# Kernel optimization log

Measured on AMD Instinct MI355X. Metric: run time of the kernel, lower is better.

Reference implementation:

```python
import jax, jax.numpy as jnp
import numpy as np

O, T = 20000, 80000
DIN_OBJ, DIN_PRED = 128, 128
H, DOUT = 256, 256
NCAPS, NHID = 8, 64
NLAYER, ROUTIT, TAU = 2, 3, 1.0
D = NCAPS * NHID                 # 512, routed feature dim
NFEAT1 = 2 * DIN_OBJ + DIN_PRED  # 384
NCLASS1 = 2 * H + DOUT           # 768
BN_EPS = 1e-5


def _l2norm(x):
    # torch fn.normalize(dim=-1): x / max(||x||, 1e-12)
    nrm = jnp.sqrt(jnp.sum(x * x, axis=-1, keepdims=True))
    return x / jnp.maximum(nrm, 1e-12)


def _rout(x, src, trg):
    # NeibRoutLayer: iterative capsule routing over edges
    n, d = x.shape
    dd = d // NCAPS
    x3 = _l2norm(x.reshape(n, NCAPS, dd))   # [n,k,dd]
    z = x3[src]                              # [m,k,dd] gathered source capsules
    u = x3
    for _ in range(ROUTIT):
        p = jax.nn.softmax(jnp.einsum('mkd,mkd->mk', z, u[trg]) / TAU, axis=1)  # [m,k]
        agg = jax.ops.segment_sum(z * p[:, :, None], trg, num_segments=n)       # scatter_add
        u = _l2norm(agg + x3)
    return u.reshape(n, d)


def _disengcn(x, src, trg, pca_w, pca_b, clf_w, clf_b, bn_g, bn_b):
    x = jax.nn.leaky_relu(x @ pca_w + pca_b)  # slope 0.01, dropout=0 (eval)
    for _ in range(NLAYER):
        x = _rout(x, src, trg)
    x = x @ clf_w + clf_b
    # BatchNorm1d in eval mode with running_mean=0, running_var=1
    x = x * (bn_g / jnp.sqrt(jnp.asarray(1.0 + BN_EPS, x.dtype))) + bn_b
    return jax.nn.leaky_relu(x)


def setup_inputs() -> dict:
    key = jax.random.key(0)
    ks = jax.random.split(key, 16)

    def unif(k, shape, stdv):
        return jax.random.uniform(k, shape, jnp.float32, -stdv, stdv)

    inp = {}
    inp['obj_vecs'] = jax.random.normal(ks[0], (O, DIN_OBJ), jnp.float32)
    inp['pred_vecs'] = jax.random.normal(ks[1], (T, DIN_PRED), jnp.float32)
    inp['edges'] = jax.random.randint(ks[2], (T, 2), 0, O, jnp.int64)
    # net1 params (SparseInputLinear uses 1/sqrt(out_dim), nn.Linear 1/sqrt(in_dim))
    inp['pca_w1'] = unif(ks[3], (NFEAT1, D), 1.0 / np.sqrt(D))
    inp['pca_b1'] = unif(ks[4], (D,), 1.0 / np.sqrt(D))
    inp['clf_w1'] = unif(ks[5], (D, NCLASS1), 1.0 / np.sqrt(D))
    inp['clf_b1'] = unif(ks[6], (NCLASS1,), 1.0 / np.sqrt(D))
    inp['bn_g1'] = 1.0 + 0.05 * jax.random.normal(ks[7], (NCLASS1,), jnp.float32)
    inp['bn_b1'] = 0.05 * jax.random.normal(ks[8], (NCLASS1,), jnp.float32)
    # net2 params
    inp['pca_w2'] = unif(ks[9], (H, D), 1.0 / np.sqrt(D))
    inp['pca_b2'] = unif(ks[10], (D,), 1.0 / np.sqrt(D))
    inp['clf_w2'] = unif(ks[11], (D, DOUT), 1.0 / np.sqrt(D))
    inp['clf_b2'] = unif(ks[12], (DOUT,), 1.0 / np.sqrt(D))
    inp['bn_g2'] = 1.0 + 0.05 * jax.random.normal(ks[13], (DOUT,), jnp.float32)
    inp['bn_b2'] = 0.05 * jax.random.normal(ks[14], (DOUT,), jnp.float32)
    return inp


def reference(obj_vecs, pred_vecs, edges, pca_w1, pca_b1, clf_w1, clf_b1, bn_g1, bn_b1,
              pca_w2, pca_b2, clf_w2, clf_b2, bn_g2, bn_b2):
    s_idx, o_idx = edges[:, 0], edges[:, 1]
    # extract_info: per-triplet concat [subj, pred, obj]
    t_vecs = jnp.concatenate([obj_vecs[s_idx], pred_vecs, obj_vecs[o_idx]], axis=1)  # [T, 384]
    out1 = _disengcn(t_vecs, s_idx, o_idx, pca_w1, pca_b1, clf_w1, clf_b1, bn_g1, bn_b1)  # [T, 768]
    # pool_objs: scatter_add subject/object features back to nodes, mean by count
    new_s = out1[:, :H]
    pred_out = out1[:, H:H + DOUT]
    new_o = out1[:, H + DOUT:]
    pooled = jax.ops.segment_sum(new_s, s_idx, num_segments=O) + \
             jax.ops.segment_sum(new_o, o_idx, num_segments=O)
    ones = jnp.ones((edges.shape[0],), out1.dtype)
    counts = jax.ops.segment_sum(ones, s_idx, num_segments=O) + \
             jax.ops.segment_sum(ones, o_idx, num_segments=O)
    pooled = pooled / jnp.maximum(counts, 1.0)[:, None]
    obj_out = _disengcn(pooled, s_idx, o_idx, pca_w2, pca_b2, clf_w2, clf_b2, bn_g2, bn_b2)  # [O, 256]
    return obj_out, pred_out
```

## Files before the change

### kernel.cpp

```cpp
#include <hip/hip_runtime.h>
#include <math.h>


#define O_N 20000
#define T_N 80000

typedef unsigned short bf_t;
typedef bf_t bfx8 __attribute__((ext_vector_type(8)));
typedef __attribute__((ext_vector_type(4))) float f32x4;
typedef __attribute__((ext_vector_type(8))) short s16x8;

#define AS1 __attribute__((address_space(1)))
#define AS3 __attribute__((address_space(3)))

__device__ __forceinline__ float leaky(float y) { return y > 0.0f ? y : 0.01f * y; }
__device__ __forceinline__ float bf2f(bf_t u) {
  union { unsigned int i; float f; } v; v.i = ((unsigned int)u) << 16; return v.f;
}
__device__ __forceinline__ bf_t f2bf(float f) {
  union { float f; unsigned int i; } v; v.f = f;
  unsigned int b = v.i;
  return (bf_t)((b + 0x7FFFu + ((b >> 16) & 1u)) >> 16);
}
__device__ __forceinline__ void gload16(const bf_t* g, bf_t* l) {
  __builtin_amdgcn_global_load_lds((const AS1 void*)g, (AS3 void*)l, 16, 0, 0);
}

__global__ void count_kernel(const int* __restrict__ edges, int* cnt_s, int* cnt_o) {
  int m = blockIdx.x * blockDim.x + threadIdx.x;
  if (m < T_N) {
    atomicAdd(&cnt_s[edges[2 * m]], 1);
    atomicAdd(&cnt_o[edges[2 * m + 1]], 1);
  }
}

__global__ void scan_kernel(const int* __restrict__ cnt_s, const int* __restrict__ cnt_o,
                            int* offs_s, int* offs_o, int* cur_o) {
  const int n = O_N;
  const int* cnt = (blockIdx.x == 0) ? cnt_s : cnt_o;
  int* offs = (blockIdx.x == 0) ? offs_s : offs_o;
  int* cur  = (blockIdx.x == 0) ? nullptr : cur_o;
  __shared__ int lds[1024];
  __shared__ int sbase;
  if (threadIdx.x == 0) sbase = 0;
  __syncthreads();
  for (int start = 0; start < n; start += 1024) {
    int i = start + (int)threadIdx.x;
    int v = (i < n) ? cnt[i] : 0;
    lds[threadIdx.x] = v;
    __syncthreads();
    for (int off = 1; off < 1024; off <<= 1) {
      int t = (threadIdx.x >= (unsigned)off) ? lds[threadIdx.x - off] : 0;
      __syncthreads();
      lds[threadIdx.x] += t;
      __syncthreads();
    }
    int base = sbase;
    int excl = base + lds[threadIdx.x] - v;
    if (i < n) { offs[i] = excl; if (cur) cur[i] = excl; }
    __syncthreads();
    if (threadIdx.x == 1023) sbase = base + lds[1023];
    __syncthreads();
  }
  if (threadIdx.x == 0) offs[n] = sbase;
}

__global__ void fill_kernel(const int* __restrict__ edges, int* cur_o, int* srcs) {
  int m = blockIdx.x * blockDim.x + threadIdx.x;
  if (m < T_N) {
    int s = edges[2 * m], o = edges[2 * m + 1];
    srcs[atomicAdd(&cur_o[o], 1)] = s;
  }
}

__global__ void transpose_cvt(const float* __restrict__ W, bf_t* __restrict__ Wt, int K, int N) {
  __shared__ float t[32][33];
  int kb = blockIdx.y << 5, nb = blockIdx.x << 5;
  int tx = threadIdx.x, ty = threadIdx.y;
#pragma unroll
  for (int r = 0; r < 32; r += 8) t[ty + r][tx] = W[(size_t)(kb + ty + r) * N + nb + tx];
  __syncthreads();
#pragma unroll
  for (int r = 0; r < 32; r += 8) Wt[(size_t)(nb + ty + r) * K + kb + tx] = f2bf(t[tx][ty + r]);
}

template <int MODE>
__global__ __launch_bounds__(256) void gemm_mfma(
    const bf_t* __restrict__ Ah, const bf_t* __restrict__ Axh,
    const float* __restrict__ Af,
    const float* __restrict__ obj, const float* __restrict__ pred,
    const int* __restrict__ edges,
    const bf_t* __restrict__ Wt, const float* __restrict__ bias,
    const float* __restrict__ bng, const float* __restrict__ bnb,
    bf_t* __restrict__ outh, float* __restrict__ outf, float* __restrict__ pool,
    int M, int N, int K) {
  constexpr bool REG = (MODE == 0 || MODE == 2);
  constexpr int ASTR = REG ? 40 : 32;
  __shared__ __align__(16) bf_t As[128 * ASTR];
  __shared__ __align__(16) bf_t Bs[128 * 32];
  __shared__ int sE[256];

  const int tid = threadIdx.x;
  const int w = tid >> 6, l = tid & 63;
  const int wr = w >> 1, wc = w & 1;
  const int row0 = blockIdx.y * 128, col0 = blockIdx.x * 128;

  const int srow = l >> 2;
  const int skb = ((l & 3) ^ ((l >> 2) & 3) ^ ((l >> 4) & 3)) * 8;
  const bf_t* pB[2];
  bf_t* ldsB[2];
  bf_t* ldsA[2];
  const bf_t* pA[2];
#pragma unroll
  for (int j = 0; j < 2; ++j) {
    int n = col0 + j * 64 + w * 16 + srow;
    pB[j] = Wt + (size_t)n * K + skb;
    ldsB[j] = Bs + (j * 64 + w * 16) * 32;
    ldsA[j] = As + (j * 64 + w * 16) * 32;
  }
  if constexpr (MODE == 1 || MODE == 3) {
#pragma unroll
    for (int j = 0; j < 2; ++j) {
      int m = row0 + j * 64 + w * 16 + srow;
      if (MODE == 3) m = min(m, M - 1);
      const bf_t* base = (MODE == 1) ? ((m < O_N) ? Ah : Axh) : Ah;
      pA[j] = base + (size_t)m * 512 + skb;
    }
  }
  int sIdx = 0, oIdx = 0, mrow = 0;
  if constexpr (MODE == 0) {
    mrow = row0 + (tid >> 1);
    sIdx = edges[2 * mrow];
    oIdx = edges[2 * mrow + 1];
  }
  if constexpr (MODE == 2) mrow = min(row0 + (tid >> 1), M - 1);
  if constexpr (MODE == 1) sE[tid] = edges[2 * row0 + tid];

  const int pkb = ((l >> 4) ^ (l & 3) ^ ((l >> 2) & 3)) * 8;
  int aoff[4], boff[4];
#pragma unroll
  for (int i = 0; i < 4; ++i) {
    int ar = wr * 64 + i * 16 + (l & 15);
    aoff[i] = REG ? (ar * 40 + (l >> 4) * 8) : (ar * 32 + pkb);
    int bn = wc * 64 + i * 16 + (l & 15);
    boff[i] = bn * 32 + pkb;
  }

  f32x4 acc[4][4];
  const f32x4 z4 = {0.f, 0.f, 0.f, 0.f};
#pragma unroll
  for (int i = 0; i < 4; ++i)
#pragma unroll
    for (int j = 0; j < 4; ++j) acc[i][j] = z4;

  for (int k0 = 0; k0 < K; k0 += 32) {
    if (k0) __syncthreads();
#pragma unroll
    for (int j = 0; j < 2; ++j) { gload16(pB[j], ldsB[j]); pB[j] += 32; }
    if constexpr (MODE == 1 || MODE == 3) {
#pragma unroll
      for (int j = 0; j < 2; ++j) { gload16(pA[j], ldsA[j]); pA[j] += 32; }
    } else {
      int r = tid >> 1, h = tid & 1;
      int c = k0 + h * 16;
      const float* base;
      if constexpr (MODE == 0) {
        if (c < 128)      base = obj  + (size_t)sIdx * 128 + c;
        else if (c < 256) base = pred + (size_t)mrow * 128 + (c - 128);
        else              base = obj  + (size_t)oIdx * 128 + (c - 256);
      } else {
        base = Af + (size_t)mrow * K + c;
      }
      float4 q0 = ((const float4*)base)[0];
      float4 q1 = ((const float4*)base)[1];
      float4 q2 = ((const float4*)base)[2];
      float4 q3 = ((const float4*)base)[3];
      bf_t* d = As + r * 40 + h * 16;
      bfx8 w0, w1;
      w0[0] = f2bf(q0.x); w0[1] = f2bf(q0.y); w0[2] = f2bf(q0.z); w0[3] = f2bf(q0.w);
      w0[4] = f2bf(q1.x); w0[5] = f2bf(q1.y); w0[6] = f2bf(q1.z); w0[7] = f2bf(q1.w);
      w1[0] = f2bf(q2.x); w1[1] = f2bf(q2.y); w1[2] = f2bf(q2.z); w1[3] = f2bf(q2.w);
      w1[4] = f2bf(q3.x); w1[5] = f2bf(q3.y); w1[6] = f2bf(q3.z); w1[7] = f2bf(q3.w);
      *(bfx8*)d = w0;
      *(bfx8*)(d + 8) = w1;
    }
    __syncthreads();
    s16x8 a[4], b[4];
#pragma unroll
    for (int i = 0; i < 4; ++i) a[i] = *(const s16x8*)(As + aoff[i]);
#pragma unroll
    for (int i = 0; i < 4; ++i) b[i] = *(const s16x8*)(Bs + boff[i]);
#pragma unroll
    for (int mi = 0; mi < 4; ++mi)
#pragma unroll
      for (int ni = 0; ni < 4; ++ni)
        acc[mi][ni] = __builtin_amdgcn_mfma_f32_16x16x32_bf16(a[mi], b[ni], acc[mi][ni], 0, 0, 0);
  }

  const int lg = l >> 4, li = l & 15;
  const float invs = 1.0f / sqrtf(1.0f + 1e-5f);
  int ncol[4];
  float bsv[4], bgv[4], bbv[4];
#pragma unroll
  for (int ni = 0; ni < 4; ++ni) {
    int n = col0 + wc * 64 + ni * 16 + li;
    ncol[ni] = n;
    bsv[ni] = bias[n];
    if constexpr (MODE == 1 || MODE == 3) { bgv[ni] = bng[n] * invs; bbv[ni] = bnb[n]; }
  }
  if constexpr (MODE == 0 || MODE == 2) {
#pragma unroll
    for (int mi = 0; mi < 4; ++mi) {
#pragma unroll
      for (int rg = 0; rg < 4; ++rg) {
        int m = row0 + wr * 64 + mi * 16 + lg * 4 + rg;
        float y[4], ssq = 0.f;
#pragma unroll
        for (int ni = 0; ni < 4; ++ni) {
          float v = leaky(acc[mi][ni][rg] + bsv[ni]);
          y[ni] = v; ssq += v * v;
        }
        ssq += __shfl_xor(ssq, 1); ssq += __shfl_xor(ssq, 2);
        ssq += __shfl_xor(ssq, 4); ssq += __shfl_xor(ssq, 8);
        if (MODE == 2 && m >= M) continue;
        float inv = 1.0f / fmaxf(sqrtf(ssq), 1e-12f);
#pragma unroll
        for (int ni = 0; ni < 4; ++ni)
          outh[(size_t)m * 512 + ncol[ni]] = f2bf(y[ni] * inv);
      }
    }
  } else if constexpr (MODE == 1) {
#pragma unroll
    for (int mi = 0; mi < 4; ++mi) {
#pragma unroll
      for (int rg = 0; rg < 4; ++rg) {
        int rloc = wr * 64 + mi * 16 + lg * 4 + rg;
        int m = row0 + rloc;
        int sI = sE[2 * rloc], oI = sE[2 * rloc + 1];
#pragma unroll
        for (int ni = 0; ni < 4; ++ni) {
          int n = ncol[ni];
          float v = leaky((acc[mi][ni][rg] + bsv[ni]) * bgv[ni] + bbv[ni]);
          if (n < 256)      atomicAdd(&pool[(size_t)sI * 256 + n], v);
          else if (n < 512) outf[(size_t)m * 256 + (n - 256)] = v;
          else              atomicAdd(&pool[(size_t)oI * 256 + (n - 512)], v);
        }
      }
    }
  } else {
#pragma unroll
    for (int mi = 0; mi < 4; ++mi) {
#pragma unroll
      for (int rg = 0; rg < 4; ++rg) {
        int m = row0 + wr * 64 + mi * 16 + lg * 4 + rg;
        if (m >= M) continue;
#pragma unroll
        for (int ni = 0; ni < 4; ++ni) {
          float v = leaky((acc[mi][ni][rg] + bsv[ni]) * bgv[ni] + bbv[ni]);
          outf[(size_t)m * 256 + ncol[ni]] = v;
        }
      }
    }
  }
}

__global__ __launch_bounds__(256) void rout_layer(
    const bf_t* __restrict__ Z, bf_t* __restrict__ U,
    const int* __restrict__ offs, const int* __restrict__ srcs, int nnodes) {
  int v = blockIdx.x * 4 + ((int)threadIdx.x >> 6);
  int lane = threadIdx.x & 63;
  if (v >= nnodes) return;
  bfx8 xv = *(const bfx8*)(Z + (size_t)v * 512 + lane * 8);
  float xr[8], ur[8];
#pragma unroll
  for (int q = 0; q < 8; ++q) { xr[q] = bf2f(xv[q]); ur[q] = xr[q]; }
  int e0 = offs[v], e1 = offs[v + 1];
  for (int it = 0; it < 3; ++it) {
    float ag[8] = {0, 0, 0, 0, 0, 0, 0, 0};
    for (int e = e0; e < e1; ++e) {
      bfx8 zv = *(const bfx8*)(Z + (size_t)srcs[e] * 512 + lane * 8);
      float zr[8];
      float d = 0.0f;
#pragma unroll
      for (int q = 0; q < 8; ++q) { zr[q] = bf2f(zv[q]); d += zr[q] * ur[q]; }
      d += __shfl_xor(d, 1); d += __shfl_xor(d, 2); d += __shfl_xor(d, 4);
      float mx = d;
      mx = fmaxf(mx, __shfl_xor(mx, 8));
      mx = fmaxf(mx, __shfl_xor(mx, 16));
      mx = fmaxf(mx, __shfl_xor(mx, 32));
      float ex = expf(d - mx);
      float sm = ex;
      sm += __shfl_xor(sm, 8); sm += __shfl_xor(sm, 16); sm += __shfl_xor(sm, 32);
      float pk = ex / sm;
#pragma unroll
      for (int q = 0; q < 8; ++q) ag[q] += pk * zr[q];
    }
    float ss = 0.0f, wv[8];
#pragma unroll
    for (int q = 0; q < 8; ++q) { wv[q] = ag[q] + xr[q]; ss += wv[q] * wv[q]; }
    ss += __shfl_xor(ss, 1); ss += __shfl_xor(ss, 2); ss += __shfl_xor(ss, 4);
    float inv = 1.0f / fmaxf(sqrtf(ss), 1e-12f);
#pragma unroll
    for (int q = 0; q < 8; ++q) ur[q] = wv[q] * inv;
  }
  bfx8 ov;
#pragma unroll
  for (int q = 0; q < 8; ++q) ov[q] = f2bf(ur[q]);
  *(bfx8*)(U + (size_t)v * 512 + lane * 8) = ov;
}

__global__ void divide_kernel(float* __restrict__ PL,
                              const int* __restrict__ offs_s, const int* __restrict__ offs_o) {
  int v = blockIdx.x;
  int c = threadIdx.x;
  float cnt = (float)((offs_s[v + 1] - offs_s[v]) + (offs_o[v + 1] - offs_o[v]));
  PL[(size_t)v * 256 + c] *= 1.0f / fmaxf(cnt, 1.0f);
}

extern "C" void kernel_launch(void* const* d_in, const int* in_sizes, int n_in,
                              void* d_out, int out_size, void* d_ws, size_t ws_size,
                              hipStream_t stream) {
  const float* obj    = (const float*)d_in[0];
  const float* pred   = (const float*)d_in[1];
  const int*   edges  = (const int*)d_in[2];
  const float* pca_w1 = (const float*)d_in[3];
  const float* pca_b1 = (const float*)d_in[4];
  const float* clf_w1 = (const float*)d_in[5];
  const float* clf_b1 = (const float*)d_in[6];
  const float* bn_g1  = (const float*)d_in[7];
  const float* bn_b1  = (const float*)d_in[8];
  const float* pca_w2 = (const float*)d_in[9];
  const float* pca_b2 = (const float*)d_in[10];
  const float* clf_w2 = (const float*)d_in[11];
  const float* clf_b2 = (const float*)d_in[12];
  const float* bn_g2  = (const float*)d_in[13];
  const float* bn_b2  = (const float*)d_in[14];
  float* outp = (float*)d_out;

  char* ws = (char*)d_ws;
  bf_t* Xh   = (bf_t*)ws;
  bf_t* Uh2  = (bf_t*)(ws + 81920000);
  float* PL  = (float*)(ws + 102400000);
  bf_t* Uh1  = (bf_t*)(ws + 102400000);
  bf_t* Wt1  = (bf_t*)(ws + 122880000);
  bf_t* Wt2  = (bf_t*)(ws + 123273216);
  bf_t* Wt3  = (bf_t*)(ws + 124059648);
  bf_t* Wt4  = (bf_t*)(ws + 124321792);
  int* I     = (int*)(ws + 124583936);
  int* cnt_s  = I;            int* cnt_o  = I + 20000;
  int* offs_s = I + 40000;    int* offs_o = I + 60001;
  int* cur_o  = I + 80002;    int* srcs   = I + 100002;

  hipMemsetAsync(cnt_s, 0, 160000, stream);
  count_kernel<<<313, 256, 0, stream>>>(edges, cnt_s, cnt_o);
  scan_kernel<<<2, 1024, 0, stream>>>(cnt_s, cnt_o, offs_s, offs_o, cur_o);
  fill_kernel<<<313, 256, 0, stream>>>(edges, cur_o, srcs);

  transpose_cvt<<<dim3(16, 12), dim3(32, 8), 0, stream>>>(pca_w1, Wt1, 384, 512);
  transpose_cvt<<<dim3(24, 16), dim3(32, 8), 0, stream>>>(clf_w1, Wt2, 512, 768);
  transpose_cvt<<<dim3(16, 8),  dim3(32, 8), 0, stream>>>(pca_w2, Wt3, 256, 512);
  transpose_cvt<<<dim3(8, 16),  dim3(32, 8), 0, stream>>>(clf_w2, Wt4, 512, 256);

  gemm_mfma<0><<<dim3(4, 625), 256, 0, stream>>>(nullptr, nullptr, nullptr, obj, pred, edges,
                                                 Wt1, pca_b1, nullptr, nullptr,
                                                 Xh, nullptr, nullptr, T_N, 512, 384);
  rout_layer<<<5000, 256, 0, stream>>>(Xh, Uh1, offs_o, srcs, O_N);
  rout_layer<<<5000, 256, 0, stream>>>(Uh1, Uh2, offs_o, srcs, O_N);
  hipMemsetAsync(PL, 0, 20480000, stream);
  gemm_mfma<1><<<dim3(6, 625), 256, 0, stream>>>(Uh2, Xh, nullptr, nullptr, nullptr, edges,
                                                 Wt2, clf_b1, bn_g1, bn_b1,
                                                 nullptr, outp + 5120000, PL, T_N, 768, 512);
  divide_kernel<<<O_N, 256, 0, stream>>>(PL, offs_s, offs_o);

  gemm_mfma<2><<<dim3(4, 157), 256, 0, stream>>>(nullptr, nullptr, PL, nullptr, nullptr, nullptr,
                                                 Wt3, pca_b2, nullptr, nullptr,
                                                 Xh, nullptr, nullptr, O_N, 512, 256);
  rout_layer<<<5000, 256, 0, stream>>>(Xh, Uh1, offs_o, srcs, O_N);
  rout_layer<<<5000, 256, 0, stream>>>(Uh1, Uh2, offs_o, srcs, O_N);
  gemm_mfma<3><<<dim3(2, 157), 256, 0, stream>>>(Uh2, nullptr, nullptr, nullptr, nullptr, nullptr,
                                                 Wt4, clf_b2, bn_g2, bn_b2,
                                                 nullptr, outp, nullptr, O_N, 256, 512);
}
```

Baseline: 773.3 us.

## Replace atomic pooling with CSR slot writes, pre-convert pred, cache rout sources

Several ideas land together. The pooling after the first DisenGCN now has the classifier GEMM write bf16 subject/object slices into CSR-ordered slots, and a gather kernel sums and averages them per node. This replaces float atomics, a memset and a divide kernel, but only when the workspace is large enough. pred_vecs is converted to bf16 once so the first GEMM can stream that segment with direct-to-LDS loads, and the register-staged A path switches to a swizzled 32-stride LDS layout. Routing caches up to 8 neighbour source rows in registers across the 3 iterations instead of re-reading them each time.

```diff
diff --git a/kernel.cpp b/kernel.cpp
--- a/kernel.cpp
+++ b/kernel.cpp
@@ -4,8 +4,10 @@
 
 #define O_N 20000
 #define T_N 80000
+#define BIG_REQ 207944000ull
 
 typedef unsigned short bf_t;
+typedef bf_t bfx4 __attribute__((ext_vector_type(4)));
 typedef bf_t bfx8 __attribute__((ext_vector_type(8)));
 typedef __attribute__((ext_vector_type(4))) float f32x4;
 typedef __attribute__((ext_vector_type(8))) short s16x8;
@@ -35,11 +37,11 @@
 }
 
 __global__ void scan_kernel(const int* __restrict__ cnt_s, const int* __restrict__ cnt_o,
-                            int* offs_s, int* offs_o, int* cur_o) {
+                            int* offs_s, int* cur_s, int* offs_o, int* cur_o) {
   const int n = O_N;
   const int* cnt = (blockIdx.x == 0) ? cnt_s : cnt_o;
   int* offs = (blockIdx.x == 0) ? offs_s : offs_o;
-  int* cur  = (blockIdx.x == 0) ? nullptr : cur_o;
+  int* cur  = (blockIdx.x == 0) ? cur_s  : cur_o;
   __shared__ int lds[1024];
   __shared__ int sbase;
   if (threadIdx.x == 0) sbase = 0;
@@ -57,7 +59,7 @@
     }
     int base = sbase;
     int excl = base + lds[threadIdx.x] - v;
-    if (i < n) { offs[i] = excl; if (cur) cur[i] = excl; }
+    if (i < n) { offs[i] = excl; cur[i] = excl; }
     __syncthreads();
     if (threadIdx.x == 1023) sbase = base + lds[1023];
     __syncthreads();
@@ -65,12 +67,28 @@
   if (threadIdx.x == 0) offs[n] = sbase;
 }
 
-__global__ void fill_kernel(const int* __restrict__ edges, int* cur_o, int* srcs) {
+__global__ void fill_kernel(const int* __restrict__ edges, int* cur_s, int* cur_o,
+                            int* srcs, int* slot_s, int* slot_o) {
   int m = blockIdx.x * blockDim.x + threadIdx.x;
   if (m < T_N) {
     int s = edges[2 * m], o = edges[2 * m + 1];
-    srcs[atomicAdd(&cur_o[o], 1)] = s;
-  }
+    int ps = atomicAdd(&cur_s[s], 1);
+    slot_s[m] = ps;
+    int po = atomicAdd(&cur_o[o], 1);
+    slot_o[m] = po;
+    srcs[po] = s;
+  }
+}
+
+__global__ void cvt_pred(const float* __restrict__ src, bf_t* __restrict__ dst, int n8) {
+  int i = blockIdx.x * blockDim.x + threadIdx.x;
+  if (i >= n8) return;
+  float4 a = ((const float4*)src)[2 * i];
+  float4 b = ((const float4*)src)[2 * i + 1];
+  bfx8 w;
+  w[0] = f2bf(a.x); w[1] = f2bf(a.y); w[2] = f2bf(a.z); w[3] = f2bf(a.w);
+  w[4] = f2bf(b.x); w[5] = f2bf(b.y); w[6] = f2bf(b.z); w[7] = f2bf(b.w);
+  *(bfx8*)(dst + (size_t)i * 8) = w;
 }
 
 __global__ void transpose_cvt(const float* __restrict__ W, bf_t* __restrict__ Wt, int K, int N) {
@@ -84,21 +102,33 @@
   for (int r = 0; r < 32; r += 8) Wt[(size_t)(nb + ty + r) * K + kb + tx] = f2bf(t[tx][ty + r]);
 }
 
+__device__ __forceinline__ void stage16(const float* base, bf_t* stA, int slot0) {
+  float4 q0 = ((const float4*)base)[0];
+  float4 q1 = ((const float4*)base)[1];
+  float4 q2 = ((const float4*)base)[2];
+  float4 q3 = ((const float4*)base)[3];
+  bfx8 w0, w1;
+  w0[0] = f2bf(q0.x); w0[1] = f2bf(q0.y); w0[2] = f2bf(q0.z); w0[3] = f2bf(q0.w);
+  w0[4] = f2bf(q1.x); w0[5] = f2bf(q1.y); w0[6] = f2bf(q1.z); w0[7] = f2bf(q1.w);
+  w1[0] = f2bf(q2.x); w1[1] = f2bf(q2.y); w1[2] = f2bf(q2.z); w1[3] = f2bf(q2.w);
+  w1[4] = f2bf(q3.x); w1[5] = f2bf(q3.y); w1[6] = f2bf(q3.z); w1[7] = f2bf(q3.w);
+  *(bfx8*)(stA + slot0 * 8) = w0;
+  *(bfx8*)(stA + (slot0 ^ 1) * 8) = w1;
+}
+
 template <int MODE>
 __global__ __launch_bounds__(256) void gemm_mfma(
     const bf_t* __restrict__ Ah, const bf_t* __restrict__ Axh,
-    const float* __restrict__ Af,
-    const float* __restrict__ obj, const float* __restrict__ pred,
+    const float* __restrict__ Af, const float* __restrict__ obj,
     const int* __restrict__ edges,
     const bf_t* __restrict__ Wt, const float* __restrict__ bias,
     const float* __restrict__ bng, const float* __restrict__ bnb,
     bf_t* __restrict__ outh, float* __restrict__ outf, float* __restrict__ pool,
+    bf_t* __restrict__ vs, bf_t* __restrict__ vo,
+    const int* __restrict__ slot_s, const int* __restrict__ slot_o,
     int M, int N, int K) {
-  constexpr bool REG = (MODE == 0 || MODE == 2);
-  constexpr int ASTR = REG ? 40 : 32;
-  __shared__ __align__(16) bf_t As[128 * ASTR];
+  __shared__ __align__(16) bf_t As[128 * 32];
   __shared__ __align__(16) bf_t Bs[128 * 32];
-  __shared__ int sE[256];
 
   const int tid = threadIdx.x;
   const int w = tid >> 6, l = tid & 63;
@@ -106,7 +136,7 @@
   const int row0 = blockIdx.y * 128, col0 = blockIdx.x * 128;
 
   const int srow = l >> 2;
-  const int skb = ((l & 3) ^ ((l >> 2) & 3) ^ ((l >> 4) & 3)) * 8;
+  const int skb = ((l & 3) ^ (srow & 3) ^ ((srow >> 2) & 3)) * 8;
   const bf_t* pB[2];
   bf_t* ldsB[2];
   bf_t* ldsA[2];
@@ -118,32 +148,35 @@
     ldsB[j] = Bs + (j * 64 + w * 16) * 32;
     ldsA[j] = As + (j * 64 + w * 16) * 32;
   }
-  if constexpr (MODE == 1 || MODE == 3) {
+  if constexpr (MODE == 1 || MODE == 3 || MODE == 4) {
 #pragma unroll
     for (int j = 0; j < 2; ++j) {
       int m = row0 + j * 64 + w * 16 + srow;
       if (MODE == 3) m = min(m, M - 1);
-      const bf_t* base = (MODE == 1) ? ((m < O_N) ? Ah : Axh) : Ah;
+      const bf_t* base = (MODE == 3) ? Ah : ((m < O_N) ? Ah : Axh);
       pA[j] = base + (size_t)m * 512 + skb;
     }
   }
+  const int r_ = tid >> 1, h_ = tid & 1;
+  const int slot0_ = (2 * h_) ^ (r_ & 3) ^ ((r_ >> 2) & 3);
+  bf_t* stA = As + r_ * 32;
   int sIdx = 0, oIdx = 0, mrow = 0;
   if constexpr (MODE == 0) {
-    mrow = row0 + (tid >> 1);
+    mrow = row0 + r_;
     sIdx = edges[2 * mrow];
     oIdx = edges[2 * mrow + 1];
-  }
-  if constexpr (MODE == 2) mrow = min(row0 + (tid >> 1), M - 1);
-  if constexpr (MODE == 1) sE[tid] = edges[2 * row0 + tid];
+#pragma unroll
+    for (int j = 0; j < 2; ++j)
+      pA[j] = Ah + (size_t)(row0 + j * 64 + w * 16 + srow) * 128 + skb;
+  }
+  if constexpr (MODE == 2) mrow = min(row0 + r_, M - 1);
 
   const int pkb = ((l >> 4) ^ (l & 3) ^ ((l >> 2) & 3)) * 8;
   int aoff[4], boff[4];
 #pragma unroll
   for (int i = 0; i < 4; ++i) {
-    int ar = wr * 64 + i * 16 + (l & 15);
-    aoff[i] = REG ? (ar * 40 + (l >> 4) * 8) : (ar * 32 + pkb);
-    int bn = wc * 64 + i * 16 + (l & 15);
-    boff[i] = bn * 32 + pkb;
+    aoff[i] = (wr * 64 + i * 16 + (l & 15)) * 32 + pkb;
+    boff[i] = (wc * 64 + i * 16 + (l & 15)) * 32 + pkb;
   }
 
   f32x4 acc[4][4];
@@ -157,32 +190,21 @@
     if (k0) __syncthreads();
 #pragma unroll
     for (int j = 0; j < 2; ++j) { gload16(pB[j], ldsB[j]); pB[j] += 32; }
-    if constexpr (MODE == 1 || MODE == 3) {
+    if constexpr (MODE == 1 || MODE == 3 || MODE == 4) {
 #pragma unroll
       for (int j = 0; j < 2; ++j) { gload16(pA[j], ldsA[j]); pA[j] += 32; }
+    } else if constexpr (MODE == 0) {
+      if (k0 >= 128 && k0 < 256) {
+        gload16(pA[0] + (k0 - 128), ldsA[0]);
+        gload16(pA[1] + (k0 - 128), ldsA[1]);
+      } else {
+        const float* base = (k0 < 128)
+            ? obj + (size_t)sIdx * 128 + k0 + h_ * 16
+            : obj + (size_t)oIdx * 128 + (k0 - 256) + h_ * 16;
+        stage16(base, stA, slot0_);
+      }
     } else {
-      int r = tid >> 1, h = tid & 1;
-      int c = k0 + h * 16;
-      const float* base;
-      if constexpr (MODE == 0) {
-        if (c < 128)      base = obj  + (size_t)sIdx * 128 + c;
-        else if (c < 256) base = pred + (size_t)mrow * 128 + (c - 128);
-        else              base = obj  + (size_t)oIdx * 128 + (c - 256);
-      } else {
-        base = Af + (size_t)mrow * K + c;
-      }
-      float4 q0 = ((const float4*)base)[0];
-      float4 q1 = ((const float4*)base)[1];
-      float4 q2 = ((const float4*)base)[2];
-      float4 q3 = ((const float4*)base)[3];
-      bf_t* d = As + r * 40 + h * 16;
-      bfx8 w0, w1;
-      w0[0] = f2bf(q0.x); w0[1] = f2bf(q0.y); w0[2] = f2bf(q0.z); w0[3] = f2bf(q0.w);
-      w0[4] = f2bf(q1.x); w0[5] = f2bf(q1.y); w0[6] = f2bf(q1.z); w0[7] = f2bf(q1.w);
-      w1[0] = f2bf(q2.x); w1[1] = f2bf(q2.y); w1[2] = f2bf(q2.z); w1[3] = f2bf(q2.w);
-      w1[4] = f2bf(q3.x); w1[5] = f2bf(q3.y); w1[6] = f2bf(q3.z); w1[7] = f2bf(q3.w);
-      *(bfx8*)d = w0;
-      *(bfx8*)(d + 8) = w1;
+      stage16(Af + (size_t)mrow * K + k0 + h_ * 16, stA, slot0_);
     }
     __syncthreads();
     s16x8 a[4], b[4];
@@ -206,7 +228,7 @@
     int n = col0 + wc * 64 + ni * 16 + li;
     ncol[ni] = n;
     bsv[ni] = bias[n];
-    if constexpr (MODE == 1 || MODE == 3) { bgv[ni] = bng[n] * invs; bbv[ni] = bnb[n]; }
+    if constexpr (MODE == 1 || MODE == 3 || MODE == 4) { bgv[ni] = bng[n] * invs; bbv[ni] = bnb[n]; }
   }
   if constexpr (MODE == 0 || MODE == 2) {
 #pragma unroll
@@ -234,9 +256,8 @@
     for (int mi = 0; mi < 4; ++mi) {
 #pragma unroll
       for (int rg = 0; rg < 4; ++rg) {
-        int rloc = wr * 64 + mi * 16 + lg * 4 + rg;
-        int m = row0 + rloc;
-        int sI = sE[2 * rloc], oI = sE[2 * rloc + 1];
+        int m = row0 + wr * 64 + mi * 16 + lg * 4 + rg;
+        int sI = edges[2 * m], oI = edges[2 * m + 1];
 #pragma unroll
         for (int ni = 0; ni < 4; ++ni) {
           int n = ncol[ni];
@@ -247,6 +268,23 @@
         }
       }
     }
+  } else if constexpr (MODE == 4) {
+#pragma unroll
+    for (int mi = 0; mi < 4; ++mi) {
+#pragma unroll
+      for (int rg = 0; rg < 4; ++rg) {
+        int m = row0 + wr * 64 + mi * 16 + lg * 4 + rg;
+        int ss = slot_s[m], so = slot_o[m];
+#pragma unroll
+        for (int ni = 0; ni < 4; ++ni) {
+          int n = ncol[ni];
+          float v = leaky((acc[mi][ni][rg] + bsv[ni]) * bgv[ni] + bbv[ni]);
+          if (n < 256)      vs[(size_t)ss * 256 + n] = f2bf(v);
+          else if (n < 512) outf[(size_t)m * 256 + (n - 256)] = v;
+          else              vo[(size_t)so * 256 + (n - 512)] = f2bf(v);
+        }
+      }
+    }
   } else {
 #pragma unroll
     for (int mi = 0; mi < 4; ++mi) {
@@ -263,6 +301,45 @@
     }
   }
 }
+
+__global__ __launch_bounds__(256) void pool_so(
+    const bf_t* __restrict__ vs, const bf_t* __restrict__ vo,
+    const int* __restrict__ offs_s, const int* __restrict__ offs_o,
+    float* __restrict__ PL, int nnodes) {
+  int v = blockIdx.x * 4 + ((int)threadIdx.x >> 6);
+  int lane = threadIdx.x & 63;
+  if (v >= nnodes) return;
+  float sx = 0, sy = 0, sz = 0, sw = 0;
+  int a0 = offs_s[v], a1 = offs_s[v + 1];
+  for (int e = a0; e < a1; ++e) {
+    bfx4 t = *(const bfx4*)(vs + (size_t)e * 256 + lane * 4);
+    sx += bf2f(t[0]); sy += bf2f(t[1]); sz += bf2f(t[2]); sw += bf2f(t[3]);
+  }
+  int b0 = offs_o[v], b1 = offs_o[v + 1];
+  for (int e = b0; e < b1; ++e) {
+    bfx4 t = *(const bfx4*)(vo + (size_t)e * 256 + lane * 4);
+    sx += bf2f(t[0]); sy += bf2f(t[1]); sz += bf2f(t[2]); sw += bf2f(t[3]);
+  }
+  float inv = 1.0f / fmaxf((float)((a1 - a0) + (b1 - b0)), 1.0f);
+  float4 r = {sx * inv, sy * inv, sz * inv, sw * inv};
+  *(float4*)(PL + (size_t)v * 256 + lane * 4) = r;
+}
+
+#define EDGE_STEP(ZR)                                                                   \
+  {                                                                                     \
+    float d = 0.0f;                                                                     \
+    _Pragma("unroll") for (int q = 0; q < 8; ++q) d += (ZR)[q] * ur[q];                 \
+    d += __shfl_xor(d, 1); d += __shfl_xor(d, 2); d += __shfl_xor(d, 4);                \
+    float mx = d;                                                                       \
+    mx = fmaxf(mx, __shfl_xor(mx, 8));                                                  \
+    mx = fmaxf(mx, __shfl_xor(mx, 16));                                                 \
+    mx = fmaxf(mx, __shfl_xor(mx, 32));                                                 \
+    float ex = expf(d - mx);                                                            \
+    float sm = ex;                                                                      \
+    sm += __shfl_xor(sm, 8); sm += __shfl_xor(sm, 16); sm += __shfl_xor(sm, 32);        \
+    float pk = ex / sm;                                                                 \
+    _Pragma("unroll") for (int q = 0; q < 8; ++q) ag[q] += pk * (ZR)[q];                \
+  }
 
 __global__ __launch_bounds__(256) void rout_layer(
     const bf_t* __restrict__ Z, bf_t* __restrict__ U,
@@ -274,34 +351,48 @@
   float xr[8], ur[8];
 #pragma unroll
   for (int q = 0; q < 8; ++q) { xr[q] = bf2f(xv[q]); ur[q] = xr[q]; }
-  int e0 = offs[v], e1 = offs[v + 1];
-  for (int it = 0; it < 3; ++it) {
-    float ag[8] = {0, 0, 0, 0, 0, 0, 0, 0};
-    for (int e = e0; e < e1; ++e) {
-      bfx8 zv = *(const bfx8*)(Z + (size_t)srcs[e] * 512 + lane * 8);
-      float zr[8];
-      float d = 0.0f;
-#pragma unroll
-      for (int q = 0; q < 8; ++q) { zr[q] = bf2f(zv[q]); d += zr[q] * ur[q]; }
-      d += __shfl_xor(d, 1); d += __shfl_xor(d, 2); d += __shfl_xor(d, 4);
-      float mx = d;
-      mx = fmaxf(mx, __shfl_xor(mx, 8));
-      mx = fmaxf(mx, __shfl_xor(mx, 16));
-      mx = fmaxf(mx, __shfl_xor(mx, 32));
-      float ex = expf(d - mx);
-      float sm = ex;
-      sm += __shfl_xor(sm, 8); sm += __shfl_xor(sm, 16); sm += __shfl_xor(sm, 32);
-      float pk = ex / sm;
-#pragma unroll
-      for (int q = 0; q < 8; ++q) ag[q] += pk * zr[q];
-    }
-    float ss = 0.0f, wv[8];
-#pragma unroll
-    for (int q = 0; q < 8; ++q) { wv[q] = ag[q] + xr[q]; ss += wv[q] * wv[q]; }
-    ss += __shfl_xor(ss, 1); ss += __shfl_xor(ss, 2); ss += __shfl_xor(ss, 4);
-    float inv = 1.0f / fmaxf(sqrtf(ss), 1e-12f);
-#pragma unroll
-    for (int q = 0; q < 8; ++q) ur[q] = wv[q] * inv;
+  int e0 = offs[v], e1 = offs[v + 1], deg = e1 - e0;
+  if (deg <= 8) {
+    bfx8 zc[8];
+#pragma unroll
+    for (int e = 0; e < 8; ++e)
+      if (e < deg) zc[e] = *(const bfx8*)(Z + (size_t)srcs[e0 + e] * 512 + lane * 8);
+    for (int it = 0; it < 3; ++it) {
+      float ag[8] = {0, 0, 0, 0, 0, 0, 0, 0};
+#pragma unroll
+      for (int e = 0; e < 8; ++e)
+        if (e < deg) {
+          float zr[8];
+#pragma unroll
+          for (int q = 0; q < 8; ++q) zr[q] = bf2f(zc[e][q]);
+          EDGE_STEP(zr);
+        }
+      float ss = 0.0f, wv[8];
+#pragma unroll
+      for (int q = 0; q < 8; ++q) { wv[q] = ag[q] + xr[q]; ss += wv[q] * wv[q]; }
+      ss += __shfl_xor(ss, 1); ss += __shfl_xor(ss, 2); ss += __shfl_xor(ss, 4);
+      float inv = 1.0f / fmaxf(sqrtf(ss), 1e-12f);
+#pragma unroll
+      for (int q = 0; q < 8; ++q) ur[q] = wv[q] * inv;
+    }
+  } else {
+    for (int it = 0; it < 3; ++it) {
+      float ag[8] = {0, 0, 0, 0, 0, 0, 0, 0};
+      for (int e = e0; e < e1; ++e) {
+        bfx8 zv = *(const bfx8*)(Z + (size_t)srcs[e] * 512 + lane * 8);
+        float zr[8];
+#pragma unroll
+        for (int q = 0; q < 8; ++q) zr[q] = bf2f(zv[q]);
+        EDGE_STEP(zr);
+      }
+      float ss = 0.0f, wv[8];
+#pragma unroll
+      for (int q = 0; q < 8; ++q) { wv[q] = ag[q] + xr[q]; ss += wv[q] * wv[q]; }
+      ss += __shfl_xor(ss, 1); ss += __shfl_xor(ss, 2); ss += __shfl_xor(ss, 4);
+      float inv = 1.0f / fmaxf(sqrtf(ss), 1e-12f);
+#pragma unroll
+      for (int q = 0; q < 8; ++q) ur[q] = wv[q] * inv;
+    }
   }
   bfx8 ov;
 #pragma unroll
@@ -338,46 +429,65 @@
   float* outp = (float*)d_out;
 
   char* ws = (char*)d_ws;
-  bf_t* Xh   = (bf_t*)ws;
-  bf_t* Uh2  = (bf_t*)(ws + 81920000);
-  float* PL  = (float*)(ws + 102400000);
-  bf_t* Uh1  = (bf_t*)(ws + 102400000);
-  bf_t* Wt1  = (bf_t*)(ws + 122880000);
-  bf_t* Wt2  = (bf_t*)(ws + 123273216);
-  bf_t* Wt3  = (bf_t*)(ws + 124059648);
-  bf_t* Wt4  = (bf_t*)(ws + 124321792);
-  int* I     = (int*)(ws + 124583936);
+  bf_t* Xh    = (bf_t*)ws;
+  bf_t* Uh2   = (bf_t*)(ws + 81920000);
+  bf_t* predh = (bf_t*)(ws + 102400000);
+  bf_t* Uh1   = (bf_t*)(ws + 102400000);
+  float* PL   = (float*)(ws + 102400000);
+  bf_t* Wt1   = (bf_t*)(ws + 122880000);
+  bf_t* Wt2   = (bf_t*)(ws + 123273216);
+  bf_t* Wt3   = (bf_t*)(ws + 124059648);
+  bf_t* Wt4   = (bf_t*)(ws + 124321792);
+  int* I      = (int*)(ws + 124583936);
   int* cnt_s  = I;            int* cnt_o  = I + 20000;
   int* offs_s = I + 40000;    int* offs_o = I + 60001;
-  int* cur_o  = I + 80002;    int* srcs   = I + 100002;
+  int* cur_s  = I + 80002;    int* cur_o  = I + 100002;
+  int* srcs   = I + 120002;
+  int* slot_s = I + 200002;   int* slot_o = I + 280002;
+  bf_t* val_s = (bf_t*)(ws + 126024000);
+  bf_t* val_o = (bf_t*)(ws + 166984000);
+  const bool big = (ws_size >= BIG_REQ);
 
   hipMemsetAsync(cnt_s, 0, 160000, stream);
   count_kernel<<<313, 256, 0, stream>>>(edges, cnt_s, cnt_o);
-  scan_kernel<<<2, 1024, 0, stream>>>(cnt_s, cnt_o, offs_s, offs_o, cur_o);
-  fill_kernel<<<313, 256, 0, stream>>>(edges, cur_o, srcs);
-
+  scan_kernel<<<2, 1024, 0, stream>>>(cnt_s, cnt_o, offs_s, cur_s, offs_o, cur_o);
+  fill_kernel<<<313, 256, 0, stream>>>(edges, cur_s, cur_o, srcs, slot_s, slot_o);
+
+  cvt_pred<<<5000, 256, 0, stream>>>(pred, predh, 1280000);
   transpose_cvt<<<dim3(16, 12), dim3(32, 8), 0, stream>>>(pca_w1, Wt1, 384, 512);
   transpose_cvt<<<dim3(24, 16), dim3(32, 8), 0, stream>>>(clf_w1, Wt2, 512, 768);
   transpose_cvt<<<dim3(16, 8),  dim3(32, 8), 0, stream>>>(pca_w2, Wt3, 256, 512);
   transpose_cvt<<<dim3(8, 16),  dim3(32, 8), 0, stream>>>(clf_w2, Wt4, 512, 256);
 
-  gemm_mfma<0><<<dim3(4, 625), 256, 0, stream>>>(nullptr, nullptr, nullptr, obj, pred, edges,
+  gemm_mfma<0><<<dim3(4, 625), 256, 0, stream>>>(predh, nullptr, nullptr, obj, edges,
                                                  Wt1, pca_b1, nullptr, nullptr,
-                                                 Xh, nullptr, nullptr, T_N, 512, 384);
+                                                 Xh, nullptr, nullptr, nullptr, nullptr,
+                                                 nullptr, nullptr, T_N, 512, 384);
   rout_layer<<<5000, 256, 0, stream>>>(Xh, Uh1, offs_o, srcs, O_N);
   rout_layer<<<5000, 256, 0, stream>>>(Uh1, Uh2, offs_o, srcs, O_N);
-  hipMemsetAsync(PL, 0, 20480000, stream);
-  gemm_mfma<1><<<dim3(6, 625), 256, 0, stream>>>(Uh2, Xh, nullptr, nullptr, nullptr, edges,
-                                                 Wt2, clf_b1, bn_g1, bn_b1,
-                                                 nullptr, outp + 5120000, PL, T_N, 768, 512);
-  divide_kernel<<<O_N, 256, 0, stream>>>(PL, offs_s, offs_o);
-
-  gemm_mfma<2><<<dim3(4, 157), 256, 0, stream>>>(nullptr, nullptr, PL, nullptr, nullptr, nullptr,
+  if (big) {
+    gemm_mfma<4><<<dim3(6, 625), 256, 0, stream>>>(Uh2, Xh, nullptr, nullptr, edges,
+                                                   Wt2, clf_b1, bn_g1, bn_b1,
+                                                   nullptr, outp + 5120000, nullptr, val_s, val_o,
+                                                   slot_s, slot_o, T_N, 768, 512);
+    pool_so<<<5000, 256, 0, stream>>>(val_s, val_o, offs_s, offs_o, PL, O_N);
+  } else {
+    hipMemsetAsync(PL, 0, 20480000, stream);
+    gemm_mfma<1><<<dim3(6, 625), 256, 0, stream>>>(Uh2, Xh, nullptr, nullptr, edges,
+                                                   Wt2, clf_b1, bn_g1, bn_b1,
+                                                   nullptr, outp + 5120000, PL, nullptr, nullptr,
+                                                   nullptr, nullptr, T_N, 768, 512);
+    divide_kernel<<<O_N, 256, 0, stream>>>(PL, offs_s, offs_o);
+  }
+
+  gemm_mfma<2><<<dim3(4, 157), 256, 0, stream>>>(nullptr, nullptr, PL, nullptr, nullptr,
                                                  Wt3, pca_b2, nullptr, nullptr,
-                                                 Xh, nullptr, nullptr, O_N, 512, 256);
+                                                 Xh, nullptr, nullptr, nullptr, nullptr,
+                                                 nullptr, nullptr, O_N, 512, 256);
   rout_layer<<<5000, 256, 0, stream>>>(Xh, Uh1, offs_o, srcs, O_N);
   rout_layer<<<5000, 256, 0, stream>>>(Uh1, Uh2, offs_o, srcs, O_N);
-  gemm_mfma<3><<<dim3(2, 157), 256, 0, stream>>>(Uh2, nullptr, nullptr, nullptr, nullptr, nullptr,
+  gemm_mfma<3><<<dim3(2, 157), 256, 0, stream>>>(Uh2, nullptr, nullptr, nullptr, nullptr,
                                                  Wt4, clf_b2, bn_g2, bn_b2,
-                                                 nullptr, outp, nullptr, O_N, 256, 512);
-}
+                                                 nullptr, outp, nullptr, nullptr, nullptr,
+                                                 nullptr, nullptr, O_N, 256, 512);
+}
```

Result: slower. 793.8 us (+2.6%).
